# Kernel optimization log

Hardware: AMD Instinct MI355X
Metric: run time of the kernel (lower is better)

The kernel has to match this reference:

```python
import jax, jax.numpy as jnp
import numpy as np

L = 8          # n_levels
F = 2          # n_features_per_level
T = 1024       # 2**log2_hashmap_size
N_MIN = 2
SCALE = 0.5
B_SCALE = np.exp(np.log(20 * SCALE / N_MIN) / (L - 1))
RES = np.floor(N_MIN * B_SCALE ** np.arange(L)).astype(np.int32)  # per-level resolution
PRIMES = np.array([1, 2654435761, 805459861], dtype=np.uint32)


def hash_grid_encode(x01, table):
    # x01: (N,3) in [0,1]; table: (L,T,F). Returns (N, L*F).
    res = jnp.asarray(RES, jnp.float32)
    pos = x01[None, :, :] * res[:, None, None]          # (L,N,3)
    f = jnp.floor(pos)
    w = pos - f                                          # trilinear weights in [0,1)
    fi = f.astype(jnp.uint32)
    primes = jnp.asarray(PRIMES)
    out = jnp.zeros((L, x01.shape[0], F), x01.dtype)
    for cx in (0, 1):
        for cy in (0, 1):
            for cz in (0, 1):
                c = jnp.asarray([cx, cy, cz], jnp.uint32)
                coords = fi + c                          # (L,N,3)
                h = (coords[..., 0] * primes[0]) ^ (coords[..., 1] * primes[1]) ^ (coords[..., 2] * primes[2])
                idx = (h & jnp.uint32(T - 1)).astype(jnp.int32)   # (L,N)
                feat = jax.vmap(lambda tab, ix: tab[ix])(table, idx)  # (L,N,F)
                wx = w[..., 0] if cx else 1.0 - w[..., 0]
                wy = w[..., 1] if cy else 1.0 - w[..., 1]
                wz = w[..., 2] if cz else 1.0 - w[..., 2]
                out = out + (wx * wy * wz)[..., None] * feat
    return jnp.transpose(out, (1, 0, 2)).reshape(x01.shape[0], L * F)


def setup_inputs() -> dict:
    key = jax.random.key(0)
    ks = jax.random.split(key, 7)
    N = 2_097_152
    x = jax.random.uniform(ks[0], (N, 3), jnp.float32) - 0.5      # in [-scale, scale]
    table = jax.random.uniform(ks[1], (L, T, F), jnp.float32, -1e-4, 1e-4)  # tcnn grid init
    def w(k, fan_in, fan_out):
        return jax.random.normal(k, (fan_in, fan_out), jnp.float32) * (1.0 / np.sqrt(fan_in))
    return {
        'x': x,
        'table': table,
        'w1': w(ks[2], 16, 64),
        'w2': w(ks[3], 64, 16),
        'r1': w(ks[4], 16, 64),
        'r2': w(ks[5], 64, 64),
        'r3': w(ks[6], 64, 1),
    }


def reference(x, table, w1, w2, r1, r2, r3):
    h = hash_grid_encode(x + SCALE, table)          # (N,16)
    # xyz_encoder MLP: 16 -> 64 (ReLU) -> 16 (linear), no biases (FullyFusedMLP)
    h = jax.nn.relu(h @ w1) @ w2                    # (N,16)
    # rgb_net: 16 -> 64 (ReLU) -> 64 (ReLU) -> 1 (Sigmoid)
    g = jax.nn.relu(h @ r1)
    g = jax.nn.relu(g @ r2)
    return jax.nn.sigmoid(g @ r3)                   # (N,1)
```

## Files before the change

### kernel.cpp

```cpp
#include <hip/hip_runtime.h>
#include <math.h>

#define NLVL 8
#define PR1 2654435761u
#define PR2 805459861u

typedef __fp16    f16x2 __attribute__((ext_vector_type(2)));
typedef _Float16  half4 __attribute__((ext_vector_type(4)));
typedef _Float16  half8 __attribute__((ext_vector_type(8)));
typedef float     floatx4 __attribute__((ext_vector_type(4)));

#define MFMA16(a,b,c) __builtin_amdgcn_mfma_f32_16x16x16f16(a,b,c,0,0,0)
#define MFMA32(a,b,c) __builtin_amdgcn_mfma_f32_16x16x32_f16(a,b,c,0,0,0)

union UH2 { unsigned u; f16x2 f; };

struct Res8 { float r[NLVL]; };

__device__ __forceinline__ unsigned pk2(float a, float b) {
    UH2 c; c.f = __builtin_amdgcn_cvt_pkrtz(a, b); return c.u;
}
__device__ __forceinline__ unsigned pkrelu(float a, float b) {
    UH2 c; c.f = __builtin_amdgcn_cvt_pkrtz(a, b);
    f16x2 z = {(__fp16)0.f, (__fp16)0.f};
    c.f = __builtin_elementwise_max(c.f, z);
    return c.u;
}
__device__ __forceinline__ half4 as_h4(uint2 u) {
    union { uint2 u; half4 h; } c; c.u = u; return c.h;
}
__device__ __forceinline__ half8 as_h8(uint4 u) {
    union { uint4 u; half8 h; } c; c.u = u; return c.h;
}
__device__ __forceinline__ f16x2 lerp2(f16x2 a, f16x2 b, f16x2 t) {
    return a + t * (b - a);
}
__device__ __forceinline__ int grow(int mo, int m) {
    return 32 * (mo >> 1) + (m >> 2) * 8 + 4 * (mo & 1) + (m & 3);
}

__global__ __launch_bounds__(512, 4)
void ngp_mfma_kernel(const float* __restrict__ x,
                     const float* __restrict__ table,
                     const float* __restrict__ w1,
                     const float* __restrict__ w2,
                     const float* __restrict__ r1,
                     const float* __restrict__ r2,
                     const float* __restrict__ r3,
                     float* __restrict__ out,
                     int N, int iters, Res8 res)
{
    __shared__ unsigned tab[NLVL * 1024];
    __shared__ __align__(16) unsigned hstg[8][384];
    __shared__ uint4    r2s4[512];

    const int tid  = threadIdx.x;
    const int lane = tid & 63, wv = tid >> 6;
    const int m16  = lane & 15, q = lane >> 4;

    {
        const float2* src = (const float2*)table;
        #pragma unroll
        for (int k = 0; k < 16; ++k) {
            int i = tid + 512 * k;
            float2 v = src[i];
            tab[i] = pk2(v.x, v.y);
        }
    }
    {
        int fid = tid >> 6, ln = tid & 63;
        int kc = fid >> 2, mo = fid & 3;
        int m = ln & 15, qq = ln >> 4;
        const float* rr = r2 + (kc * 32 + qq * 8) * 64 + mo * 16 + m;
        r2s4[tid] = make_uint4(pk2(rr[0],   rr[64]),  pk2(rr[128], rr[192]),
                               pk2(rr[256], rr[320]), pk2(rr[384], rr[448]));
    }

    half4 A1[4], A3[4];
    half8 A2[2];
    #pragma unroll
    for (int mo = 0; mo < 4; ++mo) {
        int g = grow(mo, m16);
        #pragma unroll
        for (int j = 0; j < 4; ++j) {
            int k = q * 4 + j;
            A1[mo][j] = (_Float16)w1[k * 64 + g];
            A3[mo][j] = (_Float16)r1[k * 64 + g];
        }
    }
    #pragma unroll
    for (int kc = 0; kc < 2; ++kc)
        #pragma unroll
        for (int j = 0; j < 8; ++j)
            A2[kc][j] = (_Float16)w2[(kc * 32 + q * 8 + j) * 16 + m16];
    unsigned r3p[8];
    #pragma unroll
    for (int mo = 0; mo < 4; ++mo) {
        r3p[mo * 2 + 0] = pk2(r3[mo * 16 + q * 4 + 0], r3[mo * 16 + q * 4 + 1]);
        r3p[mo * 2 + 1] = pk2(r3[mo * 16 + q * 4 + 2], r3[mo * 16 + q * 4 + 3]);
    }

    __syncthreads();

    unsigned* hs = hstg[wv];
    const char* tabb = (const char*)tab;
    const floatx4 cz = {0.f, 0.f, 0.f, 0.f};

    #pragma unroll 1
    for (int it = 0; it < iters; ++it) {
        const int pbase = (it * (int)gridDim.x + (int)blockIdx.x) * 512;
        int p = pbase + tid;

        float px = x[3 * p + 0] + 0.5f;
        float py = x[3 * p + 1] + 0.5f;
        float pz = x[3 * p + 2] + 0.5f;

        unsigned hd[8];
        #pragma unroll
        for (int l = 0; l < NLVL; ++l) {
            const float rf = res.r[l];
            float fx = px * rf, fy = py * rf, fz = pz * rf;
            float bx = floorf(fx), by = floorf(fy), bz = floorf(fz);
            UH2 wxp, wyp, wzp;
            wxp.f = __builtin_amdgcn_cvt_pkrtz(fx - bx, fx - bx);
            wyp.f = __builtin_amdgcn_cvt_pkrtz(fy - by, fy - by);
            wzp.f = __builtin_amdgcn_cvt_pkrtz(fz - bz, fz - bz);
            unsigned ix = (unsigned)bx;
            unsigned x0 = (ix << 2) & 4092u,  x1 = (x0 + 4u) & 4092u;
            unsigned y0 = (unsigned)(by * 1732.0f) & 4092u;
            unsigned y1 = (unsigned)fmaf(by, 1732.0f, 1732.0f) & 4092u;
            unsigned z0 = (unsigned)(bz * 2132.0f) & 4092u;
            unsigned z1 = (unsigned)fmaf(bz, 2132.0f, 2132.0f) & 4092u;
            unsigned a00 = x0 ^ y0, a01 = x0 ^ y1, a10 = x1 ^ y0, a11 = x1 ^ y1;
            const char* tlb = tabb + (l << 12);
            UH2 c000, c001, c010, c011, c100, c101, c110, c111;
            c000.u = *(const unsigned*)(tlb + (a00 ^ z0));
            c001.u = *(const unsigned*)(tlb + (a00 ^ z1));
            c010.u = *(const unsigned*)(tlb + (a01 ^ z0));
            c011.u = *(const unsigned*)(tlb + (a01 ^ z1));
            c100.u = *(const unsigned*)(tlb + (a10 ^ z0));
            c101.u = *(const unsigned*)(tlb + (a10 ^ z1));
            c110.u = *(const unsigned*)(tlb + (a11 ^ z0));
            c111.u = *(const unsigned*)(tlb + (a11 ^ z1));
            f16x2 zz00 = lerp2(c000.f, c001.f, wzp.f);
            f16x2 zz01 = lerp2(c010.f, c011.f, wzp.f);
            f16x2 zz10 = lerp2(c100.f, c101.f, wzp.f);
            f16x2 zz11 = lerp2(c110.f, c111.f, wzp.f);
            f16x2 yy0  = lerp2(zz00, zz01, wyp.f);
            f16x2 yy1  = lerp2(zz10, zz11, wyp.f);
            UH2 r; r.f = lerp2(yy0, yy1, wxp.f);
            hd[l] = r.u;
        }

        #pragma unroll 1
        for (int tp = 0; tp < 2; ++tp) {
            asm volatile("" ::: "memory");

            if ((q >> 1) == tp) {
                unsigned* hp = hs + ((q & 1) * 16 + m16) * 12;
                *(uint4*)&hp[0] = make_uint4(hd[0], hd[1], hd[2], hd[3]);
                *(uint4*)&hp[4] = make_uint4(hd[4], hd[5], hd[6], hd[7]);
            }

            #pragma unroll
            for (int ts = 0; ts < 2; ++ts) {
                const int t = tp * 2 + ts;
                half4 b1 = as_h4(*(const uint2*)&hs[(ts * 16 + m16) * 12 + 2 * q]);

                uint2 b2u[4];
                #pragma unroll
                for (int mo = 0; mo < 4; ++mo) {
                    floatx4 c = MFMA16(A1[mo], b1, cz);
                    b2u[mo] = make_uint2(pkrelu(c[0], c[1]), pkrelu(c[2], c[3]));
                }
                half8 bk20 = as_h8(make_uint4(b2u[0].x, b2u[0].y, b2u[1].x, b2u[1].y));
                half8 bk21 = as_h8(make_uint4(b2u[2].x, b2u[2].y, b2u[3].x, b2u[3].y));
                floatx4 c2 = MFMA32(A2[0], bk20, cz);
                c2 = MFMA32(A2[1], bk21, c2);
                half4 b3 = as_h4(make_uint2(pk2(c2[0], c2[1]), pk2(c2[2], c2[3])));

                uint2 b4u[4];
                #pragma unroll
                for (int mo = 0; mo < 4; ++mo) {
                    floatx4 c = MFMA16(A3[mo], b3, cz);
                    b4u[mo] = make_uint2(pkrelu(c[0], c[1]), pkrelu(c[2], c[3]));
                }
                half8 bk40 = as_h8(make_uint4(b4u[0].x, b4u[0].y, b4u[1].x, b4u[1].y));
                half8 bk41 = as_h8(make_uint4(b4u[2].x, b4u[2].y, b4u[3].x, b4u[3].y));
                f16x2 zacc = {(__fp16)0.f, (__fp16)0.f};
                #pragma unroll
                for (int mo = 0; mo < 4; ++mo) {
                    half8 a40 = as_h8(r2s4[(0 * 4 + mo) * 64 + lane]);
                    half8 a41 = as_h8(r2s4[(1 * 4 + mo) * 64 + lane]);
                    floatx4 c = MFMA32(a40, bk40, cz);
                    c = MFMA32(a41, bk41, c);
                    UH2 p01, p23, ra, rb;
                    p01.u = pkrelu(c[0], c[1]);
                    p23.u = pkrelu(c[2], c[3]);
                    ra.u = r3p[mo * 2 + 0]; rb.u = r3p[mo * 2 + 1];
                    zacc = zacc + p01.f * ra.f;
                    zacc = zacc + p23.f * rb.f;
                }
                float z = (float)zacc[0] + (float)zacc[1];
                z += __shfl_xor(z, 16);
                z += __shfl_xor(z, 32);
                if (lane < 16)
                    out[pbase + wv * 64 + t * 16 + lane] = 1.0f / (1.0f + __expf(-z));
            }
        }
    }
}

extern "C" void kernel_launch(void* const* d_in, const int* in_sizes, int n_in,
                              void* d_out, int out_size, void* d_ws, size_t ws_size,
                              hipStream_t stream)
{
    const float* x  = (const float*)d_in[0];
    const float* tb = (const float*)d_in[1];
    const float* w1 = (const float*)d_in[2];
    const float* w2 = (const float*)d_in[3];
    const float* r1 = (const float*)d_in[4];
    const float* r2 = (const float*)d_in[5];
    const float* r3 = (const float*)d_in[6];
    float* out = (float*)d_out;
    const int N = in_sizes[0] / 3;

    Res8 res;
    double b = exp(log(20.0 * 0.5 / 2.0) / (double)(NLVL - 1));
    for (int l = 0; l < NLVL; ++l)
        res.r[l] = (float)floor(2.0 * pow(b, (double)l));

    const int blocks = 1024, threads = 512;
    const int iters = N / (blocks * threads);
    ngp_mfma_kernel<<<blocks, threads, 0, stream>>>(x, tb, w1, w2, r1, r2, r3,
                                                    out, N, iters, res);
}
```

Before: 133.5 us.

## Replace hashed table lookup with dense per-level LUT grids in shared memory

After: 129.9 us. 1.03x faster.

```diff
diff --git a/kernel.cpp b/kernel.cpp
--- a/kernel.cpp
+++ b/kernel.cpp
@@ -14,8 +14,6 @@
 #define MFMA32(a,b,c) __builtin_amdgcn_mfma_f32_16x16x32_f16(a,b,c,0,0,0)
 
 union UH2 { unsigned u; f16x2 f; };
-
-struct Res8 { float r[NLVL]; };
 
 __device__ __forceinline__ unsigned pk2(float a, float b) {
     UH2 c; c.f = __builtin_amdgcn_cvt_pkrtz(a, b); return c.u;
@@ -39,7 +37,55 @@
     return 32 * (mo >> 1) + (m >> 2) * 8 + 4 * (mo & 1) + (m & 3);
 }
 
-__global__ __launch_bounds__(512, 4)
+template<int S, int BASE, int LVL>
+__device__ __forceinline__ void build_lut(unsigned* tab, const float2* __restrict__ src,
+                                          int tid) {
+    constexpr int SZ = S * S * S;
+    for (int e = tid; e < SZ; e += 512) {
+        int z  = e / (S * S);
+        int r  = e - z * (S * S);
+        int y  = r / S;
+        int xg = r - y * S;
+        unsigned h = ((unsigned)xg ^ ((unsigned)y * PR1) ^ ((unsigned)z * PR2)) & 1023u;
+        float2 v = src[LVL * 1024 + h];
+        tab[BASE + e] = pk2(v.x, v.y);
+    }
+}
+
+template<int S, int OFF>
+__device__ __forceinline__ unsigned trilerp(const unsigned* __restrict__ t,
+                                            f16x2 wx, f16x2 wy, f16x2 wz) {
+    UH2 c000, c100, c010, c110, c001, c101, c011, c111;
+    c000.u = t[OFF + 0];             c100.u = t[OFF + 1];
+    c010.u = t[OFF + S];             c110.u = t[OFF + S + 1];
+    c001.u = t[OFF + S * S];         c101.u = t[OFF + S * S + 1];
+    c011.u = t[OFF + S * S + S];     c111.u = t[OFF + S * S + S + 1];
+    f16x2 a0 = lerp2(c000.f, c100.f, wx);
+    f16x2 a1 = lerp2(c010.f, c110.f, wx);
+    f16x2 a2 = lerp2(c001.f, c101.f, wx);
+    f16x2 a3 = lerp2(c011.f, c111.f, wx);
+    f16x2 b0 = lerp2(a0, a1, wy);
+    f16x2 b1 = lerp2(a2, a3, wy);
+    UH2 r; r.f = lerp2(b0, b1, wz);
+    return r.u;
+}
+
+template<int S>
+__device__ __forceinline__ unsigned gidx(float px, float py, float pz,
+                                         f16x2& wx, f16x2& wy, f16x2& wz) {
+    const float rf = (float)(S - 1);
+    float fx = px * rf, fy = py * rf, fz = pz * rf;
+    float bx = floorf(fx), by = floorf(fy), bz = floorf(fz);
+    UH2 a, b, c;
+    a.f = __builtin_amdgcn_cvt_pkrtz(fx - bx, fx - bx);
+    b.f = __builtin_amdgcn_cvt_pkrtz(fy - by, fy - by);
+    c.f = __builtin_amdgcn_cvt_pkrtz(fz - bz, fz - bz);
+    wx = a.f; wy = b.f; wz = c.f;
+    return (unsigned)fmaf(bz, (float)(S * S), fmaf(by, (float)S, bx));
+}
+
+template<int R7>
+__global__ __launch_bounds__(512, 8)
 void ngp_mfma_kernel(const float* __restrict__ x,
                      const float* __restrict__ table,
                      const float* __restrict__ w1,
@@ -48,9 +94,10 @@
                      const float* __restrict__ r2,
                      const float* __restrict__ r3,
                      float* __restrict__ out,
-                     int N, int iters, Res8 res)
+                     int iters)
 {
-    __shared__ unsigned tab[NLVL * 1024];
+    constexpr int S7 = R7 + 1;
+    __shared__ unsigned tab[1253 + S7 * S7 * S7];
     __shared__ __align__(16) unsigned hstg[8][384];
     __shared__ uint4    r2s4[512];
 
@@ -60,12 +107,14 @@
 
     {
         const float2* src = (const float2*)table;
-        #pragma unroll
-        for (int k = 0; k < 16; ++k) {
-            int i = tid + 512 * k;
-            float2 v = src[i];
-            tab[i] = pk2(v.x, v.y);
-        }
+        build_lut<3,    0, 0>(tab, src, tid);
+        build_lut<3,   27, 1>(tab, src, tid);
+        build_lut<4,   54, 2>(tab, src, tid);
+        build_lut<4,  118, 3>(tab, src, tid);
+        build_lut<6,  182, 4>(tab, src, tid);
+        build_lut<7,  398, 5>(tab, src, tid);
+        build_lut<8,  741, 6>(tab, src, tid);
+        build_lut<S7,1253, 7>(tab, src, tid);
     }
     {
         int fid = tid >> 6, ln = tid & 63;
@@ -103,7 +152,6 @@
     __syncthreads();
 
     unsigned* hs = hstg[wv];
-    const char* tabb = (const char*)tab;
     const floatx4 cz = {0.f, 0.f, 0.f, 0.f};
 
     #pragma unroll 1
@@ -116,40 +164,24 @@
         float pz = x[3 * p + 2] + 0.5f;
 
         unsigned hd[8];
-        #pragma unroll
-        for (int l = 0; l < NLVL; ++l) {
-            const float rf = res.r[l];
-            float fx = px * rf, fy = py * rf, fz = pz * rf;
-            float bx = floorf(fx), by = floorf(fy), bz = floorf(fz);
-            UH2 wxp, wyp, wzp;
-            wxp.f = __builtin_amdgcn_cvt_pkrtz(fx - bx, fx - bx);
-            wyp.f = __builtin_amdgcn_cvt_pkrtz(fy - by, fy - by);
-            wzp.f = __builtin_amdgcn_cvt_pkrtz(fz - bz, fz - bz);
-            unsigned ix = (unsigned)bx;
-            unsigned x0 = (ix << 2) & 4092u,  x1 = (x0 + 4u) & 4092u;
-            unsigned y0 = (unsigned)(by * 1732.0f) & 4092u;
-            unsigned y1 = (unsigned)fmaf(by, 1732.0f, 1732.0f) & 4092u;
-            unsigned z0 = (unsigned)(bz * 2132.0f) & 4092u;
-            unsigned z1 = (unsigned)fmaf(bz, 2132.0f, 2132.0f) & 4092u;
-            unsigned a00 = x0 ^ y0, a01 = x0 ^ y1, a10 = x1 ^ y0, a11 = x1 ^ y1;
-            const char* tlb = tabb + (l << 12);
-            UH2 c000, c001, c010, c011, c100, c101, c110, c111;
-            c000.u = *(const unsigned*)(tlb + (a00 ^ z0));
-            c001.u = *(const unsigned*)(tlb + (a00 ^ z1));
-            c010.u = *(const unsigned*)(tlb + (a01 ^ z0));
-            c011.u = *(const unsigned*)(tlb + (a01 ^ z1));
-            c100.u = *(const unsigned*)(tlb + (a10 ^ z0));
-            c101.u = *(const unsigned*)(tlb + (a10 ^ z1));
-            c110.u = *(const unsigned*)(tlb + (a11 ^ z0));
-            c111.u = *(const unsigned*)(tlb + (a11 ^ z1));
-            f16x2 zz00 = lerp2(c000.f, c001.f, wzp.f);
-            f16x2 zz01 = lerp2(c010.f, c011.f, wzp.f);
-            f16x2 zz10 = lerp2(c100.f, c101.f, wzp.f);
-            f16x2 zz11 = lerp2(c110.f, c111.f, wzp.f);
-            f16x2 yy0  = lerp2(zz00, zz01, wyp.f);
-            f16x2 yy1  = lerp2(zz10, zz11, wyp.f);
-            UH2 r; r.f = lerp2(yy0, yy1, wxp.f);
-            hd[l] = r.u;
+        {
+            f16x2 wx, wy, wz;
+            unsigned i = gidx<3>(px, py, pz, wx, wy, wz);
+            const unsigned* t = tab + i;
+            hd[0] = trilerp<3,  0>(t, wx, wy, wz);
+            hd[1] = trilerp<3, 27>(t, wx, wy, wz);
+            i = gidx<4>(px, py, pz, wx, wy, wz);
+            t = tab + 54 + i;
+            hd[2] = trilerp<4,  0>(t, wx, wy, wz);
+            hd[3] = trilerp<4, 64>(t, wx, wy, wz);
+            i = gidx<6>(px, py, pz, wx, wy, wz);
+            hd[4] = trilerp<6, 0>(tab + 182 + i, wx, wy, wz);
+            i = gidx<7>(px, py, pz, wx, wy, wz);
+            hd[5] = trilerp<7, 0>(tab + 398 + i, wx, wy, wz);
+            i = gidx<8>(px, py, pz, wx, wy, wz);
+            hd[6] = trilerp<8, 0>(tab + 741 + i, wx, wy, wz);
+            i = gidx<S7>(px, py, pz, wx, wy, wz);
+            hd[7] = trilerp<S7, 0>(tab + 1253 + i, wx, wy, wz);
         }
 
         #pragma unroll 1
@@ -225,13 +257,15 @@
     float* out = (float*)d_out;
     const int N = in_sizes[0] / 3;
 
-    Res8 res;
     double b = exp(log(20.0 * 0.5 / 2.0) / (double)(NLVL - 1));
-    for (int l = 0; l < NLVL; ++l)
-        res.r[l] = (float)floor(2.0 * pow(b, (double)l));
+    int r7 = (int)floor(2.0 * pow(b, 7.0));
 
     const int blocks = 1024, threads = 512;
     const int iters = N / (blocks * threads);
-    ngp_mfma_kernel<<<blocks, threads, 0, stream>>>(x, tb, w1, w2, r1, r2, r3,
-                                                    out, N, iters, res);
-}
+    if (r7 == 9)
+        ngp_mfma_kernel<9><<<blocks, threads, 0, stream>>>(x, tb, w1, w2, r1, r2, r3,
+                                                           out, iters);
+    else
+        ngp_mfma_kernel<10><<<blocks, threads, 0, stream>>>(x, tb, w1, w2, r1, r2, r3,
+                                                            out, iters);
+}
```
